# Performance work log

Hardware: AMD Instinct MI355X
Metric: run time of the kernel (lower is better)

Reference implementation:

```python
import jax, jax.numpy as jnp
import numpy as np

B, T, I, H, O = 256, 2048, 6, 64, 6  # batch, time, input_dim, hidden_dim, output_dim


def setup_inputs() -> dict:
    key = jax.random.key(0)
    ks = jax.random.split(key, 11)
    s = 0.1  # param init scale
    return {
        "x": jax.random.normal(ks[0], (B, T, I), jnp.float32),
        # LSTM layer 0 (gate order i, f, g, o as in PyTorch; b = b_ih + b_hh)
        "Wih0": jax.random.normal(ks[1], (4 * H, I), jnp.float32) * s,
        "Whh0": jax.random.normal(ks[2], (4 * H, H), jnp.float32) * s,
        "b0": jax.random.normal(ks[3], (4 * H,), jnp.float32) * s,
        # LSTM layer 1
        "Wih1": jax.random.normal(ks[4], (4 * H, H), jnp.float32) * s,
        "Whh1": jax.random.normal(ks[5], (4 * H, H), jnp.float32) * s,
        "b1": jax.random.normal(ks[6], (4 * H,), jnp.float32) * s,
        # FC head
        "W1": jax.random.normal(ks[7], (H, H), jnp.float32) * s,
        "bf1": jax.random.normal(ks[8], (H,), jnp.float32) * s,
        "W2": jax.random.normal(ks[9], (O, H), jnp.float32) * s,
        "bf2": jax.random.normal(ks[10], (O,), jnp.float32) * s,
    }


def lstm_layer(x, Wih, Whh, b):
    """Single LSTM layer, batch_first. x: (B, T, F) -> (B, T, H)."""
    h_dim = Whh.shape[1]
    # precompute input contribution to gates for all timesteps: (B, T, 4H)
    xg = jnp.einsum('btf,gf->btg', x, Wih) + b

    def step(carry, xg_t):
        h, c = carry
        g = xg_t + h @ Whh.T                      # (B, 4H)
        i, f, gg, o = jnp.split(g, 4, axis=-1)    # PyTorch gate order i,f,g,o
        i = jax.nn.sigmoid(i)
        f = jax.nn.sigmoid(f)
        gg = jnp.tanh(gg)
        o = jax.nn.sigmoid(o)
        c = f * c + i * gg
        h = o * jnp.tanh(c)
        return (h, c), h

    h0 = jnp.zeros((x.shape[0], h_dim), x.dtype)
    _, hs = jax.lax.scan(step, (h0, h0), jnp.swapaxes(xg, 0, 1))  # (T, B, H)
    return jnp.swapaxes(hs, 0, 1)


def reference(x, Wih0, Whh0, b0, Wih1, Whh1, b1, W1, bf1, W2, bf2):
    h = lstm_layer(x, Wih0, Whh0, b0)
    h = lstm_layer(h, Wih1, Whh1, b1)   # eval mode: inter-layer dropout disabled
    h = jax.nn.relu(h @ W1.T + bf1)
    return h @ W2.T + bf2               # (B, T, O)
```

## Files before the change

kernel.cpp:

```cpp
#include <hip/hip_runtime.h>

#define TT 2048
#define HH 64
#define II 6
#define OO 6
#define NTHR 512

typedef float    f32x4 __attribute__((ext_vector_type(4)));
typedef _Float16 f16x8 __attribute__((ext_vector_type(8)));

__device__ __forceinline__ float fast_sig(float v) {
    return __builtin_amdgcn_rcpf(1.0f + __expf(-v));
}
__device__ __forceinline__ float fast_tanh(float v) {
    return 1.0f - 2.0f * __builtin_amdgcn_rcpf(__expf(2.0f * v) + 1.0f);
}

#define MFMA(a, b, c) __builtin_amdgcn_mfma_f32_16x16x32_f16((a), (b), (c), 0, 0, 0)

__global__
__attribute__((amdgpu_flat_work_group_size(NTHR, NTHR)))
__attribute__((amdgpu_waves_per_eu(2, 2)))
void lstm_mfma_kernel(const float* __restrict__ x,
                      const float* __restrict__ Wih0, const float* __restrict__ Whh0,
                      const float* __restrict__ b0,
                      const float* __restrict__ Wih1, const float* __restrict__ Whh1,
                      const float* __restrict__ b1,
                      const float* __restrict__ W1, const float* __restrict__ bf1,
                      const float* __restrict__ W2, const float* __restrict__ bf2,
                      float* __restrict__ out)
{
    const int row  = blockIdx.x;
    const int tid  = threadIdx.x;
    const int wid  = tid >> 6;
    const int lane = tid & 63;
    const int n    = lane & 15;
    const int q    = lane >> 4;
    const bool isA = wid < 4;
    const int  w   = isA ? wid : wid - 4;

    __shared__ __attribute__((aligned(16))) _Float16 H0[2][HH];
    __shared__ __attribute__((aligned(16))) _Float16 H1[2][HH];
    __shared__ __attribute__((aligned(16))) _Float16 Rb[2][HH];
    __shared__ __attribute__((aligned(16))) _Float16 Xb[2][32];
    __shared__ __attribute__((aligned(16))) float    XG[2][256];

    if (tid < HH) {
        H0[0][tid] = (_Float16)0.f; H0[1][tid] = (_Float16)0.f;
        H1[0][tid] = (_Float16)0.f; H1[1][tid] = (_Float16)0.f;
        Rb[0][tid] = (_Float16)0.f; Rb[1][tid] = (_Float16)0.f;
    }
    if (tid < 32) { Xb[0][tid] = (_Float16)0.f; Xb[1][tid] = (_Float16)0.f; }
    if (tid < 256) { XG[0][tid] = 0.f; XG[1][tid] = 0.f; }

    f16x8 frag[20];
    float bias[8];
    #pragma unroll
    for (int i = 0; i < 8; ++i) bias[i] = 0.f;

    auto mk = [&](const float* W, int r, int ld, int kbase, int kmax, bool rok) {
        f16x8 f;
        #pragma unroll
        for (int i = 0; i < 8; ++i) {
            int kk = kbase + 8 * q + i;
            f[i] = (rok && kk < kmax) ? (_Float16)W[r * ld + kk] : (_Float16)0.f;
        }
        return f;
    };

    if (isA) {
        #pragma unroll
        for (int g = 0; g < 4; ++g) {
            const int r0 = g * HH + 16 * w + n;
            frag[g * 3 + 0] = mk(Whh0, r0, HH, 0,  HH, true);
            frag[g * 3 + 1] = mk(Whh0, r0, HH, 32, HH, true);
            frag[g * 3 + 2] = mk(Wih0, r0, II, 0,  II, true);
            bias[g] = b0[r0];
            const int r1 = 16 * (4 * g + w) + n;
            frag[12 + g * 2 + 0] = mk(Wih1, r1, HH, 0,  HH, true);
            frag[12 + g * 2 + 1] = mk(Wih1, r1, HH, 32, HH, true);
            bias[4 + g] = b1[r1];
        }
    } else {
        #pragma unroll
        for (int g = 0; g < 4; ++g) {
            const int r0 = g * HH + 16 * w + n;
            frag[g * 2 + 0] = mk(Whh1, r0, HH, 0,  HH, true);
            frag[g * 2 + 1] = mk(Whh1, r0, HH, 32, HH, true);
        }
        const int rf = 16 * w + n;
        frag[8]  = mk(W1, rf, HH, 0,  HH, true);
        frag[9]  = mk(W1, rf, HH, 32, HH, true);
        bias[0] = bf1[rf];
        frag[10] = mk(W2, n, HH, 0,  HH, n < OO);
        frag[11] = mk(W2, n, HH, 32, HH, n < OO);
        bias[1] = (n < OO) ? bf2[n] : 0.f;
        #pragma unroll
        for (int i = 12; i < 20; ++i) frag[i] = frag[0];
    }

    const float* xrow   = x   + (size_t)row * TT * II;
    float*       outrow = out + (size_t)row * TT * OO;

    if (tid < II) Xb[0][tid] = (_Float16)xrow[tid];

    float cst = 0.f;
    __syncthreads();

    for (int t = 0; t <= TT + 3; ++t) {
        const int slp = (t + 1) & 1;
        const int slc = t & 1;

        if (isA) {
            const f16x8 a0 = *reinterpret_cast<const f16x8*>(&H0[slp][8 * q]);
            const f16x8 a1 = *reinterpret_cast<const f16x8*>(&H0[slp][32 + 8 * q]);
            const f16x8 a2 = *reinterpret_cast<const f16x8*>(&Xb[slc][8 * q]);
            f32x4 d0, d1, d2, d3;
            #pragma unroll
            for (int g = 0; g < 4; ++g) {
                f32x4 acc = {bias[g], bias[g], bias[g], bias[g]};
                acc = MFMA(a0, frag[g * 3 + 0], acc);
                acc = MFMA(a1, frag[g * 3 + 1], acc);
                acc = MFMA(a2, frag[g * 3 + 2], acc);
                if (g == 0) d0 = acc; else if (g == 1) d1 = acc;
                else if (g == 2) d2 = acc; else d3 = acc;
                f32x4 ae = {bias[4 + g], bias[4 + g], bias[4 + g], bias[4 + g]};
                ae = MFMA(a0, frag[12 + g * 2 + 0], ae);
                ae = MFMA(a1, frag[12 + g * 2 + 1], ae);
                if (lane < 16) XG[slp][16 * (4 * g + w) + lane] = ae[0];
            }
            if (t < TT) {
                float i_ = fast_sig(d0[0]), f_ = fast_sig(d1[0]);
                float g_ = fast_tanh(d2[0]), o_ = fast_sig(d3[0]);
                cst = f_ * cst + i_ * g_;
                float h = o_ * fast_tanh(cst);
                if (lane < 16) H0[slc][16 * w + lane] = (_Float16)h;
            }
            if (wid == 0 && lane < II && t + 1 < TT)
                Xb[slp][lane] = (_Float16)xrow[(size_t)(t + 1) * II + lane];
        } else {
            const int s2 = t - 2, s3 = t - 3, s4 = t - 4;
            const f16x8 a0 = *reinterpret_cast<const f16x8*>(&H1[slp][8 * q]);
            const f16x8 a1 = *reinterpret_cast<const f16x8*>(&H1[slp][32 + 8 * q]);
            f32x4 d0, d1, d2, d3;
            #pragma unroll
            for (int g = 0; g < 4; ++g) {
                const float xg = XG[slc][16 * (4 * g + w) + n];
                f32x4 acc = {xg, xg, xg, xg};
                acc = MFMA(a0, frag[g * 2 + 0], acc);
                acc = MFMA(a1, frag[g * 2 + 1], acc);
                if (g == 0) d0 = acc; else if (g == 1) d1 = acc;
                else if (g == 2) d2 = acc; else d3 = acc;
            }
            if (s2 >= 0 && s2 < TT) {
                float i_ = fast_sig(d0[0]), f_ = fast_sig(d1[0]);
                float g_ = fast_tanh(d2[0]), o_ = fast_sig(d3[0]);
                cst = f_ * cst + i_ * g_;
                float h = o_ * fast_tanh(cst);
                if (lane < 16) H1[slc][16 * w + lane] = (_Float16)h;
            }
            {
                f32x4 acc = {bias[0], bias[0], bias[0], bias[0]};
                acc = MFMA(a0, frag[8], acc);
                acc = MFMA(a1, frag[9], acc);
                if (s3 >= 0 && s3 < TT && lane < 16)
                    Rb[slp][16 * w + lane] = (_Float16)fmaxf(acc[0], 0.f);
            }
            if (w == 0) {
                const f16x8 r0 = *reinterpret_cast<const f16x8*>(&Rb[slc][8 * q]);
                const f16x8 r1 = *reinterpret_cast<const f16x8*>(&Rb[slc][32 + 8 * q]);
                f32x4 acc = {bias[1], bias[1], bias[1], bias[1]};
                acc = MFMA(r0, frag[10], acc);
                acc = MFMA(r1, frag[11], acc);
                if (s4 >= 0 && s4 < TT && lane < OO)
                    outrow[(size_t)s4 * OO + lane] = acc[0];
            }
        }
        __syncthreads();
    }
}

extern "C" void kernel_launch(void* const* d_in, const int* in_sizes, int n_in,
                              void* d_out, int out_size, void* d_ws, size_t ws_size,
                              hipStream_t stream) {
    const float* xp   = (const float*)d_in[0];
    const float* Wih0 = (const float*)d_in[1];
    const float* Whh0 = (const float*)d_in[2];
    const float* b0   = (const float*)d_in[3];
    const float* Wih1 = (const float*)d_in[4];
    const float* Whh1 = (const float*)d_in[5];
    const float* b1   = (const float*)d_in[6];
    const float* W1   = (const float*)d_in[7];
    const float* bf1  = (const float*)d_in[8];
    const float* W2   = (const float*)d_in[9];
    const float* bf2  = (const float*)d_in[10];
    float* outp = (float*)d_out;

    lstm_mfma_kernel<<<dim3(256), dim3(NTHR), 0, stream>>>(
        xp, Wih0, Whh0, b0, Wih1, Whh1, b1, W1, bf1, W2, bf2, outp);
}
```

Before: 1.215 ms.

## Batch 16 sequences per block so MFMA N dimension covers real batch rows

Each block now processes 16 batch rows instead of one, using the MFMA's 16-wide dimension for batch rather than wasting 15 of 16 columns. Layer-1 input projection moves to the B waves and the FC1 head moves to the A waves, and H0 gets a 4-deep buffer to support the rebalanced pipeline. The grid shrinks from 256 to 16 blocks, leaving most CUs idle, and __syncthreads is replaced by a hand-written lgkmcnt wait plus s_barrier. The intent is to amortize per-step latency across 16 rows, at the cost of much lower parallelism across the GPU.

```diff
diff --git a/kernel.cpp b/kernel.cpp
--- a/kernel.cpp
+++ b/kernel.cpp
@@ -4,10 +4,14 @@
 #define HH 64
 #define II 6
 #define OO 6
+#define MB 16
 #define NTHR 512
 
 typedef float    f32x4 __attribute__((ext_vector_type(4)));
+typedef float    f32x2 __attribute__((ext_vector_type(2)));
 typedef _Float16 f16x8 __attribute__((ext_vector_type(8)));
+typedef _Float16 f16x4 __attribute__((ext_vector_type(4)));
+typedef _Float16 f16x2 __attribute__((ext_vector_type(2)));
 
 __device__ __forceinline__ float fast_sig(float v) {
     return __builtin_amdgcn_rcpf(1.0f + __expf(-v));
@@ -17,6 +21,7 @@
 }
 
 #define MFMA(a, b, c) __builtin_amdgcn_mfma_f32_16x16x32_f16((a), (b), (c), 0, 0, 0)
+#define LGKM_BARRIER() asm volatile("s_waitcnt lgkmcnt(0)\ns_barrier" ::: "memory")
 
 __global__
 __attribute__((amdgpu_flat_work_group_size(NTHR, NTHR)))
@@ -30,33 +35,30 @@
                       const float* __restrict__ W2, const float* __restrict__ bf2,
                       float* __restrict__ out)
 {
-    const int row  = blockIdx.x;
+    const int row0 = blockIdx.x * MB;
     const int tid  = threadIdx.x;
     const int wid  = tid >> 6;
     const int lane = tid & 63;
     const int n    = lane & 15;
     const int q    = lane >> 4;
     const bool isA = wid < 4;
-    const int  w   = isA ? wid : wid - 4;
-
-    __shared__ __attribute__((aligned(16))) _Float16 H0[2][HH];
-    __shared__ __attribute__((aligned(16))) _Float16 H1[2][HH];
-    __shared__ __attribute__((aligned(16))) _Float16 Rb[2][HH];
-    __shared__ __attribute__((aligned(16))) _Float16 Xb[2][32];
-    __shared__ __attribute__((aligned(16))) float    XG[2][256];
-
-    if (tid < HH) {
-        H0[0][tid] = (_Float16)0.f; H0[1][tid] = (_Float16)0.f;
-        H1[0][tid] = (_Float16)0.f; H1[1][tid] = (_Float16)0.f;
-        Rb[0][tid] = (_Float16)0.f; Rb[1][tid] = (_Float16)0.f;
-    }
-    if (tid < 32) { Xb[0][tid] = (_Float16)0.f; Xb[1][tid] = (_Float16)0.f; }
-    if (tid < 256) { XG[0][tid] = 0.f; XG[1][tid] = 0.f; }
-
-    f16x8 frag[20];
-    float bias[8];
-    #pragma unroll
-    for (int i = 0; i < 8; ++i) bias[i] = 0.f;
+    const int  w   = wid & 3;
+
+    __shared__ __attribute__((aligned(16))) _Float16 H0[4][1024];
+    __shared__ __attribute__((aligned(16))) _Float16 H1[2][1024];
+    __shared__ __attribute__((aligned(16))) _Float16 Rb[2][1024];
+    __shared__ __attribute__((aligned(16))) _Float16 XT[2][128];
+
+    {
+        _Float16* p = &H0[0][0];
+        for (int i = tid; i < 4 * 1024; i += NTHR) p[i] = (_Float16)0.f;
+        p = &H1[0][0];
+        for (int i = tid; i < 2 * 1024; i += NTHR) p[i] = (_Float16)0.f;
+        p = &Rb[0][0];
+        for (int i = tid; i < 2 * 1024; i += NTHR) p[i] = (_Float16)0.f;
+        p = &XT[0][0];
+        for (int i = tid; i < 2 * 128; i += NTHR) p[i] = (_Float16)0.f;
+    }
 
     auto mk = [&](const float* W, int r, int ld, int kbase, int kmax, bool rok) {
         f16x8 f;
@@ -67,116 +69,202 @@
         }
         return f;
     };
+    const f32x4 zero4 = {0.f, 0.f, 0.f, 0.f};
+    f16x8 zero8;
+    #pragma unroll
+    for (int i = 0; i < 8; ++i) zero8[i] = (_Float16)0.f;
+
+    f16x8 FR[18];
+    #pragma unroll
+    for (int i = 0; i < 18; ++i) FR[i] = zero8;
+    f32x4 biasv[4] = {zero4, zero4, zero4, zero4};
+    f32x4 biasF = zero4;
 
     if (isA) {
         #pragma unroll
         for (int g = 0; g < 4; ++g) {
             const int r0 = g * HH + 16 * w + n;
-            frag[g * 3 + 0] = mk(Whh0, r0, HH, 0,  HH, true);
-            frag[g * 3 + 1] = mk(Whh0, r0, HH, 32, HH, true);
-            frag[g * 3 + 2] = mk(Wih0, r0, II, 0,  II, true);
-            bias[g] = b0[r0];
-            const int r1 = 16 * (4 * g + w) + n;
-            frag[12 + g * 2 + 0] = mk(Wih1, r1, HH, 0,  HH, true);
-            frag[12 + g * 2 + 1] = mk(Wih1, r1, HH, 32, HH, true);
-            bias[4 + g] = b1[r1];
-        }
+            FR[2 * g + 0] = mk(Whh0, r0, HH, 0,  HH, true);
+            FR[2 * g + 1] = mk(Whh0, r0, HH, 32, HH, true);
+            FR[8 + g]     = mk(Wih0, r0, II, 0,  II, true);
+            const int u = g * HH + 16 * w + 4 * q;
+            biasv[g] = f32x4{b0[u], b0[u + 1], b0[u + 2], b0[u + 3]};
+        }
+        FR[12] = mk(W1, 16 * w + n, HH, 0,  HH, true);
+        FR[13] = mk(W1, 16 * w + n, HH, 32, HH, true);
+        const int uf = 16 * w + 4 * q;
+        biasF = f32x4{bf1[uf], bf1[uf + 1], bf1[uf + 2], bf1[uf + 3]};
     } else {
         #pragma unroll
         for (int g = 0; g < 4; ++g) {
             const int r0 = g * HH + 16 * w + n;
-            frag[g * 2 + 0] = mk(Whh1, r0, HH, 0,  HH, true);
-            frag[g * 2 + 1] = mk(Whh1, r0, HH, 32, HH, true);
-        }
-        const int rf = 16 * w + n;
-        frag[8]  = mk(W1, rf, HH, 0,  HH, true);
-        frag[9]  = mk(W1, rf, HH, 32, HH, true);
-        bias[0] = bf1[rf];
-        frag[10] = mk(W2, n, HH, 0,  HH, n < OO);
-        frag[11] = mk(W2, n, HH, 32, HH, n < OO);
-        bias[1] = (n < OO) ? bf2[n] : 0.f;
-        #pragma unroll
-        for (int i = 12; i < 20; ++i) frag[i] = frag[0];
-    }
-
-    const float* xrow   = x   + (size_t)row * TT * II;
-    float*       outrow = out + (size_t)row * TT * OO;
-
-    if (tid < II) Xb[0][tid] = (_Float16)xrow[tid];
-
-    float cst = 0.f;
+            FR[4 * g + 0] = mk(Wih1, r0, HH, 0,  HH, true);
+            FR[4 * g + 1] = mk(Wih1, r0, HH, 32, HH, true);
+            FR[4 * g + 2] = mk(Whh1, r0, HH, 0,  HH, true);
+            FR[4 * g + 3] = mk(Whh1, r0, HH, 32, HH, true);
+            const int u = g * HH + 16 * w + 4 * q;
+            biasv[g] = f32x4{b1[u], b1[u + 1], b1[u + 2], b1[u + 3]};
+        }
+        if (w == 0) {
+            FR[16] = mk(W2, n, HH, 0,  HH, n < OO);
+            FR[17] = mk(W2, n, HH, 32, HH, n < OO);
+            #pragma unroll
+            for (int r2 = 0; r2 < 4; ++r2) {
+                const int u = 4 * q + r2;
+                biasF[r2] = (u < OO) ? bf2[u] : 0.f;
+            }
+        }
+    }
+
+    const float* xpl = nullptr;
+    if (wid == 7 && lane < MB) {
+        const float* p = x + (size_t)(row0 + lane) * TT * II;
+        unsigned long long pp = (unsigned long long)p;
+        asm volatile("" : "+v"(pp));
+        xpl = (const float*)pp;
+        f32x2 u0 = *(const f32x2*)(xpl + 0);
+        f32x2 u1 = *(const f32x2*)(xpl + 2);
+        f32x2 u2 = *(const f32x2*)(xpl + 4);
+        *(f16x4*)&XT[0][lane * 8] =
+            f16x4{(_Float16)u0[0], (_Float16)u0[1], (_Float16)u1[0], (_Float16)u1[1]};
+        *(f16x2*)&XT[0][lane * 8 + 4] = f16x2{(_Float16)u2[0], (_Float16)u2[1]};
+    }
+
+    float* outbase = out + (size_t)row0 * TT * OO;
+    f32x4 cst = zero4;
+
     __syncthreads();
 
     for (int t = 0; t <= TT + 3; ++t) {
-        const int slp = (t + 1) & 1;
-        const int slc = t & 1;
+        const int s0r = (t + 3) & 3, s0w = t & 3, s0b = (t + 2) & 3;
+        const int sp = (t + 1) & 1, sc = t & 1;
 
         if (isA) {
-            const f16x8 a0 = *reinterpret_cast<const f16x8*>(&H0[slp][8 * q]);
-            const f16x8 a1 = *reinterpret_cast<const f16x8*>(&H0[slp][32 + 8 * q]);
-            const f16x8 a2 = *reinterpret_cast<const f16x8*>(&Xb[slc][8 * q]);
+            const f16x8 ha0 = *(const f16x8*)&H0[s0r][q * 128 + n * 8];
+            const f16x8 ha1 = *(const f16x8*)&H0[s0r][(4 + q) * 128 + n * 8];
+            f16x8 xb = zero8;
+            if (q == 0) xb = *(const f16x8*)&XT[sc][n * 8];
+            const f16x8 hb0 = *(const f16x8*)&H1[sp][q * 128 + n * 8];
+            const f16x8 hb1 = *(const f16x8*)&H1[sp][(4 + q) * 128 + n * 8];
+
             f32x4 d0, d1, d2, d3;
-            #pragma unroll
-            for (int g = 0; g < 4; ++g) {
-                f32x4 acc = {bias[g], bias[g], bias[g], bias[g]};
-                acc = MFMA(a0, frag[g * 3 + 0], acc);
-                acc = MFMA(a1, frag[g * 3 + 1], acc);
-                acc = MFMA(a2, frag[g * 3 + 2], acc);
-                if (g == 0) d0 = acc; else if (g == 1) d1 = acc;
-                else if (g == 2) d2 = acc; else d3 = acc;
-                f32x4 ae = {bias[4 + g], bias[4 + g], bias[4 + g], bias[4 + g]};
-                ae = MFMA(a0, frag[12 + g * 2 + 0], ae);
-                ae = MFMA(a1, frag[12 + g * 2 + 1], ae);
-                if (lane < 16) XG[slp][16 * (4 * g + w) + lane] = ae[0];
+            {
+                f32x4 p0 = MFMA(FR[0], ha0, biasv[0]);
+                f32x4 p1 = MFMA(FR[1], ha1, zero4);
+                f32x4 p2 = MFMA(FR[8], xb, zero4);
+                d0 = (p0 + p1) + p2;
+                p0 = MFMA(FR[2], ha0, biasv[1]);
+                p1 = MFMA(FR[3], ha1, zero4);
+                p2 = MFMA(FR[9], xb, zero4);
+                d1 = (p0 + p1) + p2;
+                p0 = MFMA(FR[4], ha0, biasv[2]);
+                p1 = MFMA(FR[5], ha1, zero4);
+                p2 = MFMA(FR[10], xb, zero4);
+                d2 = (p0 + p1) + p2;
+                p0 = MFMA(FR[6], ha0, biasv[3]);
+                p1 = MFMA(FR[7], ha1, zero4);
+                p2 = MFMA(FR[11], xb, zero4);
+                d3 = (p0 + p1) + p2;
+            }
+            f32x4 f0 = MFMA(FR[12], hb0, biasF);
+            f32x4 f1 = MFMA(FR[13], hb1, zero4);
+            f32x4 fr = f0 + f1;
+
+            if (t >= 3 && t < TT + 3) {
+                f16x4 rv = {(_Float16)fmaxf(fr[0], 0.f), (_Float16)fmaxf(fr[1], 0.f),
+                            (_Float16)fmaxf(fr[2], 0.f), (_Float16)fmaxf(fr[3], 0.f)};
+                *(f16x4*)&Rb[sp][(2 * w + (q >> 1)) * 128 + n * 8 + (q & 1) * 4] = rv;
             }
             if (t < TT) {
-                float i_ = fast_sig(d0[0]), f_ = fast_sig(d1[0]);
-                float g_ = fast_tanh(d2[0]), o_ = fast_sig(d3[0]);
-                cst = f_ * cst + i_ * g_;
-                float h = o_ * fast_tanh(cst);
-                if (lane < 16) H0[slc][16 * w + lane] = (_Float16)h;
-            }
-            if (wid == 0 && lane < II && t + 1 < TT)
-                Xb[slp][lane] = (_Float16)xrow[(size_t)(t + 1) * II + lane];
+                float hv[4];
+                #pragma unroll
+                for (int r2 = 0; r2 < 4; ++r2) {
+                    float i_ = fast_sig(d0[r2]), f_ = fast_sig(d1[r2]);
+                    float g_ = fast_tanh(d2[r2]), o_ = fast_sig(d3[r2]);
+                    cst[r2] = f_ * cst[r2] + i_ * g_;
+                    hv[r2] = o_ * fast_tanh(cst[r2]);
+                }
+                f16x4 hh = {(_Float16)hv[0], (_Float16)hv[1],
+                            (_Float16)hv[2], (_Float16)hv[3]};
+                *(f16x4*)&H0[s0w][(2 * w + (q >> 1)) * 128 + n * 8 + (q & 1) * 4] = hh;
+            }
         } else {
-            const int s2 = t - 2, s3 = t - 3, s4 = t - 4;
-            const f16x8 a0 = *reinterpret_cast<const f16x8*>(&H1[slp][8 * q]);
-            const f16x8 a1 = *reinterpret_cast<const f16x8*>(&H1[slp][32 + 8 * q]);
+            f32x2 u0, u1, u2;
+            if (wid == 7 && lane < MB) {
+                const int tn = (t + 1 < TT) ? t + 1 : TT - 1;
+                const float* xp2 = xpl + (size_t)tn * II;
+                u0 = *(const f32x2*)(xp2 + 0);
+                u1 = *(const f32x2*)(xp2 + 2);
+                u2 = *(const f32x2*)(xp2 + 4);
+            }
+            const f16x8 h00 = *(const f16x8*)&H0[s0b][q * 128 + n * 8];
+            const f16x8 h01 = *(const f16x8*)&H0[s0b][(4 + q) * 128 + n * 8];
+            const f16x8 a0  = *(const f16x8*)&H1[sp][q * 128 + n * 8];
+            const f16x8 a1  = *(const f16x8*)&H1[sp][(4 + q) * 128 + n * 8];
+
             f32x4 d0, d1, d2, d3;
-            #pragma unroll
-            for (int g = 0; g < 4; ++g) {
-                const float xg = XG[slc][16 * (4 * g + w) + n];
-                f32x4 acc = {xg, xg, xg, xg};
-                acc = MFMA(a0, frag[g * 2 + 0], acc);
-                acc = MFMA(a1, frag[g * 2 + 1], acc);
-                if (g == 0) d0 = acc; else if (g == 1) d1 = acc;
-                else if (g == 2) d2 = acc; else d3 = acc;
-            }
+            {
+                f32x4 p0 = MFMA(FR[0], h00, biasv[0]);
+                f32x4 p1 = MFMA(FR[1], h01, zero4);
+                f32x4 p2 = MFMA(FR[2], a0, zero4);
+                f32x4 p3 = MFMA(FR[3], a1, zero4);
+                d0 = (p0 + p1) + (p2 + p3);
+                p0 = MFMA(FR[4], h00, biasv[1]);
+                p1 = MFMA(FR[5], h01, zero4);
+                p2 = MFMA(FR[6], a0, zero4);
+                p3 = MFMA(FR[7], a1, zero4);
+                d1 = (p0 + p1) + (p2 + p3);
+                p0 = MFMA(FR[8], h00, biasv[2]);
+                p1 = MFMA(FR[9], h01, zero4);
+                p2 = MFMA(FR[10], a0, zero4);
+                p3 = MFMA(FR[11], a1, zero4);
+                d2 = (p0 + p1) + (p2 + p3);
+                p0 = MFMA(FR[12], h00, biasv[3]);
+                p1 = MFMA(FR[13], h01, zero4);
+                p2 = MFMA(FR[14], a0, zero4);
+                p3 = MFMA(FR[15], a1, zero4);
+                d3 = (p0 + p1) + (p2 + p3);
+            }
+            const int s2 = t - 2;
             if (s2 >= 0 && s2 < TT) {
-                float i_ = fast_sig(d0[0]), f_ = fast_sig(d1[0]);
-                float g_ = fast_tanh(d2[0]), o_ = fast_sig(d3[0]);
-                cst = f_ * cst + i_ * g_;
-                float h = o_ * fast_tanh(cst);
-                if (lane < 16) H1[slc][16 * w + lane] = (_Float16)h;
-            }
-            {
-                f32x4 acc = {bias[0], bias[0], bias[0], bias[0]};
-                acc = MFMA(a0, frag[8], acc);
-                acc = MFMA(a1, frag[9], acc);
-                if (s3 >= 0 && s3 < TT && lane < 16)
-                    Rb[slp][16 * w + lane] = (_Float16)fmaxf(acc[0], 0.f);
+                float hv[4];
+                #pragma unroll
+                for (int r2 = 0; r2 < 4; ++r2) {
+                    float i_ = fast_sig(d0[r2]), f_ = fast_sig(d1[r2]);
+                    float g_ = fast_tanh(d2[r2]), o_ = fast_sig(d3[r2]);
+                    cst[r2] = f_ * cst[r2] + i_ * g_;
+                    hv[r2] = o_ * fast_tanh(cst[r2]);
+                }
+                f16x4 hh = {(_Float16)hv[0], (_Float16)hv[1],
+                            (_Float16)hv[2], (_Float16)hv[3]};
+                *(f16x4*)&H1[sc][(2 * w + (q >> 1)) * 128 + n * 8 + (q & 1) * 4] = hh;
             }
             if (w == 0) {
-                const f16x8 r0 = *reinterpret_cast<const f16x8*>(&Rb[slc][8 * q]);
-                const f16x8 r1 = *reinterpret_cast<const f16x8*>(&Rb[slc][32 + 8 * q]);
-                f32x4 acc = {bias[1], bias[1], bias[1], bias[1]};
-                acc = MFMA(r0, frag[10], acc);
-                acc = MFMA(r1, frag[11], acc);
-                if (s4 >= 0 && s4 < TT && lane < OO)
-                    outrow[(size_t)s4 * OO + lane] = acc[0];
-            }
-        }
-        __syncthreads();
+                const f16x8 r0 = *(const f16x8*)&Rb[sc][q * 128 + n * 8];
+                const f16x8 r1 = *(const f16x8*)&Rb[sc][(4 + q) * 128 + n * 8];
+                f32x4 o0 = MFMA(FR[16], r0, biasF);
+                f32x4 o1 = MFMA(FR[17], r1, zero4);
+                f32x4 ov = o0 + o1;
+                const int s4 = t - 4;
+                if (s4 >= 0 && s4 < TT) {
+                    float* po = outbase + (size_t)n * TT * OO + (size_t)s4 * OO;
+                    if (q == 0) {
+                        *(f32x2*)(po + 0) = f32x2{ov[0], ov[1]};
+                        *(f32x2*)(po + 2) = f32x2{ov[2], ov[3]};
+                    } else if (q == 1) {
+                        *(f32x2*)(po + 4) = f32x2{ov[0], ov[1]};
+                    }
+                }
+            }
+            if (wid == 7 && lane < MB) {
+                *(f16x4*)&XT[sp][lane * 8] =
+                    f16x4{(_Float16)u0[0], (_Float16)u0[1],
+                          (_Float16)u1[0], (_Float16)u1[1]};
+                *(f16x2*)&XT[sp][lane * 8 + 4] =
+                    f16x2{(_Float16)u2[0], (_Float16)u2[1]};
+            }
+        }
+        LGKM_BARRIER();
     }
 }
 
@@ -196,6 +284,6 @@
     const float* bf2  = (const float*)d_in[10];
     float* outp = (float*)d_out;
 
-    lstm_mfma_kernel<<<dim3(256), dim3(NTHR), 0, stream>>>(
+    lstm_mfma_kernel<<<dim3(256 / MB), dim3(NTHR), 0, stream>>>(
         xp, Wih0, Whh0, b0, Wih1, Whh1, b1, W1, bf1, W2, bf2, outp);
 }
```

Result: slower. 2.214 ms (+82.2%).
